# Performance work log

Measured on AMD Instinct MI355X. Metric: run time of the kernel, lower is better.

## Reference

```python
import jax, jax.numpy as jnp
import numpy as np

B, S, E = 8, 2048, 1024
H, DK = 128, 8  # embed_dim = H * DK; DK = n_wires per quantum head


def setup_inputs() -> dict:
    key = jax.random.key(0)
    k1, k2, k3, k4 = jax.random.split(key, 4)
    x = jax.random.normal(k1, (B, S, E), dtype=jnp.float32)
    theta = jax.random.normal(k2, (H, DK), dtype=jnp.float32)  # trainable RX angles per head/wire
    W = jax.random.normal(k3, (E, E), dtype=jnp.float32) * (1.0 / np.sqrt(E))
    b = jax.random.normal(k4, (E,), dtype=jnp.float32) * 0.01
    return {"x": x, "theta": theta, "W": W, "b": b}


def reference(x, theta, W, b):
    # Quantum circuit per token/head: RX(x_i) then RX(theta_i) on wire i starting
    # from |0...0>. Single-qubit RX gates compose: RX(a)RX(b)=RX(a+b), and
    # <Z> after RX(angle)|0> = cos(angle). So the MeasureAll(PauliZ) output is
    # cos(x_i + theta_i) elementwise -- fully vectorized over batch/seq/head/wire.
    Bx, Sx, Ex = x.shape
    Hx, dk = theta.shape
    xs = x.reshape(Bx, Sx, Hx, dk)            # [B,S,H,dk]
    head_out = jnp.cos(xs + theta[None, None])  # [B,S,H,dk]
    out = head_out.reshape(Bx, Sx, Ex)
    return out @ W.T + b                       # combine Linear
```

## Files before the change

### kernel.cpp

```cpp
#include <hip/hip_runtime.h>
#include <hip/hip_bf16.h>
#include <stdint.h>

#define M_DIM 16384
#define N_DIM 1024
#define K_DIM 1024

typedef __attribute__((ext_vector_type(8))) short short8;
typedef __attribute__((ext_vector_type(4))) float f32x4;

#define GLD_LDS(g, l) __builtin_amdgcn_global_load_lds( \
    (const __attribute__((address_space(1))) unsigned int*)(g), \
    (__attribute__((address_space(3))) unsigned int*)(l), 16, 0, 0)

__device__ __forceinline__ unsigned short f2bf(float f) {
  union { float f; unsigned int u; } v;
  v.f = f;
  unsigned int u = v.u + 0x7FFFu + ((v.u >> 16) & 1u);
  return (unsigned short)(u >> 16);
}

#define PREP_A_BLOCKS (M_DIM * K_DIM / (256 * 8))
#define PREP_W_BLOCKS (N_DIM * K_DIM / (256 * 8))
__global__ __launch_bounds__(256) void prep_all(const float* __restrict__ x,
                                                const float* __restrict__ theta,
                                                const float* __restrict__ W,
                                                unsigned short* __restrict__ A,
                                                unsigned short* __restrict__ Wb) {
  if (blockIdx.x < PREP_A_BLOCKS) {
    const long i = ((long)blockIdx.x * 256 + threadIdx.x) * 8;
    const int k = (int)(i & (K_DIM - 1));
    float4 x0 = *(const float4*)(x + i);
    float4 x1 = *(const float4*)(x + i + 4);
    float4 t0 = *(const float4*)(theta + k);
    float4 t1 = *(const float4*)(theta + k + 4);
    union { unsigned short s[8]; short8 v; } o;
    o.s[0] = f2bf(__cosf(x0.x + t0.x));
    o.s[1] = f2bf(__cosf(x0.y + t0.y));
    o.s[2] = f2bf(__cosf(x0.z + t0.z));
    o.s[3] = f2bf(__cosf(x0.w + t0.w));
    o.s[4] = f2bf(__cosf(x1.x + t1.x));
    o.s[5] = f2bf(__cosf(x1.y + t1.y));
    o.s[6] = f2bf(__cosf(x1.z + t1.z));
    o.s[7] = f2bf(__cosf(x1.w + t1.w));
    *(short8*)(A + i) = o.v;
  } else {
    const long i = ((long)(blockIdx.x - PREP_A_BLOCKS) * 256 + threadIdx.x) * 8;
    float4 w0 = *(const float4*)(W + i);
    float4 w1 = *(const float4*)(W + i + 4);
    union { unsigned short s[8]; short8 v; } o;
    o.s[0] = f2bf(w0.x); o.s[1] = f2bf(w0.y); o.s[2] = f2bf(w0.z); o.s[3] = f2bf(w0.w);
    o.s[4] = f2bf(w1.x); o.s[5] = f2bf(w1.y); o.s[6] = f2bf(w1.z); o.s[7] = f2bf(w1.w);
    *(short8*)(Wb + i) = o.v;
  }
}

__global__ __launch_bounds__(512, 2) void gemm_bt(const unsigned short* __restrict__ A,
                                                  const unsigned short* __restrict__ Bt,
                                                  const float* __restrict__ bias,
                                                  float* __restrict__ C) {
  constexpr int NTT = K_DIM / 64;
  __shared__ unsigned short As[4 * 8192];
  __shared__ unsigned short Bs[4 * 8192];
  const int tid = threadIdx.x;

  const int L = blockIdx.y * 4 + blockIdx.x;
  const int xcd = L & 7;
  const int idx = L >> 3;
  const int by = xcd * 8 + (idx >> 2);
  const int bx = idx & 3;
  const int m0 = by * 256;
  const int n0 = bx * 256;

  const int lane = tid & 63;
  const int wave = tid >> 6;
  const int wm = (wave >> 2) * 128;
  const int wn = (wave & 3) * 64;
  const int fr = lane & 15;
  const int fq = lane >> 4;

  f32x4 acc[8][4] = {};

  const int srow = ((tid >> 5) << 3) | (tid & 7);
  const int kc = (tid >> 3) & 3;
  const unsigned short* AgU = A + (long)(m0 + srow) * K_DIM + kc * 8;
  const unsigned short* BgU = Bt + (long)(n0 + srow) * K_DIM + kc * 8;
  unsigned short* AsD = As + tid * 8;
  unsigned short* BsD = Bs + tid * 8;

#define STAGE_A(UNIT, TAU, KH) do { \
    const unsigned short* g_ = AgU + (TAU) * 64 + (KH) * 32; \
    unsigned short* d_ = AsD + (UNIT) * 8192; \
    GLD_LDS(g_, d_); \
    GLD_LDS(g_ + (long)128 * K_DIM, d_ + 4096); \
  } while (0)
#define STAGE_B(UNIT, TAU, KH) do { \
    const unsigned short* g_ = BgU + (TAU) * 64 + (KH) * 32; \
    unsigned short* d_ = BsD + (UNIT) * 8192; \
    GLD_LDS(g_, d_); \
    GLD_LDS(g_ + (long)128 * K_DIM, d_ + 4096); \
  } while (0)

  const int baseA = ((wm >> 3) + (fr >> 3)) * 256 + fq * 64 + (fr & 7) * 8;
  const int baseB = ((wn >> 3) + (fr >> 3)) * 256 + fq * 64 + (fr & 7) * 8;

  short8 bf0, bf1, bf2, bf3;

#define MFMA16(IH, A0, A1, A2, A3) do { \
    __builtin_amdgcn_s_setprio(1); \
    acc[(IH)*4+0][0] = __builtin_amdgcn_mfma_f32_16x16x32_bf16(A0, bf0, acc[(IH)*4+0][0], 0, 0, 0); \
    acc[(IH)*4+0][1] = __builtin_amdgcn_mfma_f32_16x16x32_bf16(A0, bf1, acc[(IH)*4+0][1], 0, 0, 0); \
    acc[(IH)*4+0][2] = __builtin_amdgcn_mfma_f32_16x16x32_bf16(A0, bf2, acc[(IH)*4+0][2], 0, 0, 0); \
    acc[(IH)*4+0][3] = __builtin_amdgcn_mfma_f32_16x16x32_bf16(A0, bf3, acc[(IH)*4+0][3], 0, 0, 0); \
    acc[(IH)*4+1][0] = __builtin_amdgcn_mfma_f32_16x16x32_bf16(A1, bf0, acc[(IH)*4+1][0], 0, 0, 0); \
    acc[(IH)*4+1][1] = __builtin_amdgcn_mfma_f32_16x16x32_bf16(A1, bf1, acc[(IH)*4+1][1], 0, 0, 0); \
    acc[(IH)*4+1][2] = __builtin_amdgcn_mfma_f32_16x16x32_bf16(A1, bf2, acc[(IH)*4+1][2], 0, 0, 0); \
    acc[(IH)*4+1][3] = __builtin_amdgcn_mfma_f32_16x16x32_bf16(A1, bf3, acc[(IH)*4+1][3], 0, 0, 0); \
    acc[(IH)*4+2][0] = __builtin_amdgcn_mfma_f32_16x16x32_bf16(A2, bf0, acc[(IH)*4+2][0], 0, 0, 0); \
    acc[(IH)*4+2][1] = __builtin_amdgcn_mfma_f32_16x16x32_bf16(A2, bf1, acc[(IH)*4+2][1], 0, 0, 0); \
    acc[(IH)*4+2][2] = __builtin_amdgcn_mfma_f32_16x16x32_bf16(A2, bf2, acc[(IH)*4+2][2], 0, 0, 0); \
    acc[(IH)*4+2][3] = __builtin_amdgcn_mfma_f32_16x16x32_bf16(A2, bf3, acc[(IH)*4+2][3], 0, 0, 0); \
    acc[(IH)*4+3][0] = __builtin_amdgcn_mfma_f32_16x16x32_bf16(A3, bf0, acc[(IH)*4+3][0], 0, 0, 0); \
    acc[(IH)*4+3][1] = __builtin_amdgcn_mfma_f32_16x16x32_bf16(A3, bf1, acc[(IH)*4+3][1], 0, 0, 0); \
    acc[(IH)*4+3][2] = __builtin_amdgcn_mfma_f32_16x16x32_bf16(A3, bf2, acc[(IH)*4+3][2], 0, 0, 0); \
    acc[(IH)*4+3][3] = __builtin_amdgcn_mfma_f32_16x16x32_bf16(A3, bf3, acc[(IH)*4+3][3], 0, 0, 0); \
    __builtin_amdgcn_s_setprio(0); \
  } while (0)

#define BAR() do { asm volatile("" ::: "memory"); __builtin_amdgcn_s_barrier(); \
                   asm volatile("" ::: "memory"); } while (0)
#define VMW(N) asm volatile("s_waitcnt vmcnt(" #N ")" ::: "memory")

#define PHASE_LO(Au, Bu, ISSUE, WAIT) do { \
    BAR(); \
    ISSUE; \
    bf0 = *(const short8*)((Bu) + baseB + 0); \
    bf1 = *(const short8*)((Bu) + baseB + 512); \
    bf2 = *(const short8*)((Bu) + baseB + 1024); \
    bf3 = *(const short8*)((Bu) + baseB + 1536); \
    { short8 a0 = *(const short8*)((Au) + baseA + 0); \
      short8 a1 = *(const short8*)((Au) + baseA + 512); \
      short8 a2 = *(const short8*)((Au) + baseA + 1024); \
      short8 a3 = *(const short8*)((Au) + baseA + 1536); \
      MFMA16(0, a0, a1, a2, a3); } \
    WAIT; \
  } while (0)

#define PHASE_HI(Au, ISSUE, WAIT) do { \
    BAR(); \
    ISSUE; \
    { short8 a0 = *(const short8*)((Au) + baseA + 2048); \
      short8 a1 = *(const short8*)((Au) + baseA + 2560); \
      short8 a2 = *(const short8*)((Au) + baseA + 3072); \
      short8 a3 = *(const short8*)((Au) + baseA + 3584); \
      MFMA16(1, a0, a1, a2, a3); } \
    WAIT; \
  } while (0)

  STAGE_A(0, 0, 0);
  STAGE_B(0, 0, 0);
  STAGE_A(1, 0, 1);
  STAGE_B(1, 0, 1);
  STAGE_A(2, 1, 0);
  STAGE_B(2, 1, 0);
  VMW(8);

  for (int t = 0; t < NTT - 2; ++t) {
    const int db = t & 1;
    const int u0 = db * 2;
    const int u1 = db * 2 + 1;
    const int v1 = (db ^ 1) * 2 + 1;
    const unsigned short* Au0 = As + u0 * 8192;
    const unsigned short* Bu0 = Bs + u0 * 8192;
    const unsigned short* Au1 = As + u1 * 8192;
    const unsigned short* Bu1 = Bs + u1 * 8192;
    PHASE_LO(Au0, Bu0, STAGE_A(v1, t + 1, 1), (void)0);
    PHASE_HI(Au0,      STAGE_B(v1, t + 1, 1), VMW(8));
    PHASE_LO(Au1, Bu1, STAGE_A(u0, t + 2, 0), (void)0);
    PHASE_HI(Au1,      STAGE_B(u0, t + 2, 0), VMW(8));
  }
  {
    const unsigned short* Au0 = As;
    const unsigned short* Bu0 = Bs;
    const unsigned short* Au1 = As + 8192;
    const unsigned short* Bu1 = Bs + 8192;
    PHASE_LO(Au0, Bu0, STAGE_A(3, 15, 1), (void)0);
    PHASE_HI(Au0,      STAGE_B(3, 15, 1), VMW(8));
    PHASE_LO(Au1, Bu1, (void)0,           (void)0);
    PHASE_HI(Au1,      (void)0,           VMW(4));
  }
  {
    const unsigned short* Au0 = As + 2 * 8192;
    const unsigned short* Bu0 = Bs + 2 * 8192;
    const unsigned short* Au1 = As + 3 * 8192;
    const unsigned short* Bu1 = Bs + 3 * 8192;
    PHASE_LO(Au0, Bu0, (void)0, (void)0);
    PHASE_HI(Au0,      (void)0, VMW(0));
    PHASE_LO(Au1, Bu1, (void)0, (void)0);
    PHASE_HI(Au1,      (void)0, (void)0);
  }

  const int cn = lane & 15;
  const int rq = (lane >> 4) * 4;
#pragma unroll
  for (int j = 0; j < 4; ++j) {
    const int n = n0 + wn + j * 16 + cn;
    const float bv = bias[n];
#pragma unroll
    for (int i = 0; i < 8; ++i) {
      const long mb = (long)(m0 + wm + i * 16 + rq) * N_DIM + n;
#pragma unroll
      for (int r = 0; r < 4; ++r)
        C[mb + (long)r * N_DIM] = acc[i][j][r] + bv;
    }
  }
}

extern "C" void kernel_launch(void* const* d_in, const int* in_sizes, int n_in,
                              void* d_out, int out_size, void* d_ws, size_t ws_size,
                              hipStream_t stream) {
  const float* x = (const float*)d_in[0];
  const float* theta = (const float*)d_in[1];
  const float* W = (const float*)d_in[2];
  const float* b = (const float*)d_in[3];
  float* out = (float*)d_out;

  unsigned short* Abf = (unsigned short*)d_ws;
  unsigned short* Wbf = Abf + (size_t)M_DIM * K_DIM;

  hipLaunchKernelGGL(prep_all, dim3(PREP_A_BLOCKS + PREP_W_BLOCKS), dim3(256), 0,
                     stream, x, theta, W, Abf, Wbf);
  hipLaunchKernelGGL(gemm_bt, dim3(N_DIM / 256, M_DIM / 256), dim3(512), 0, stream,
                     Abf, Wbf, b, out);
}
```

Before: 160.0 us.

## Issue LDS fragment reads before barrier and reorder B/A staging

Each phase now reads its A/B fragments from LDS and issues the next global-to-LDS stage before the workgroup barrier, then waits on lgkmcnt and runs the MFMAs after the barrier. The aim is to overlap LDS read latency with barrier wait and keep memory traffic flowing. The staging order is swapped so B is issued before A, which changes which buffer the vmcnt waits cover. This reorders the read/write hazards across buffers, so correctness depends on the staged buffer not aliasing the one being read in the same phase.

```diff
diff --git a/kernel.cpp b/kernel.cpp
--- a/kernel.cpp
+++ b/kernel.cpp
@@ -130,40 +130,45 @@
 #define BAR() do { asm volatile("" ::: "memory"); __builtin_amdgcn_s_barrier(); \
                    asm volatile("" ::: "memory"); } while (0)
 #define VMW(N) asm volatile("s_waitcnt vmcnt(" #N ")" ::: "memory")
-
-#define PHASE_LO(Au, Bu, ISSUE, WAIT) do { \
-    BAR(); \
-    ISSUE; \
+#define LGKM0() do { asm volatile("s_waitcnt lgkmcnt(0)" ::: "memory"); \
+                     __builtin_amdgcn_sched_barrier(0); } while (0)
+
+#define PHASE_LO(Au, Bu, ISSUE, WAITPRE) do { \
     bf0 = *(const short8*)((Bu) + baseB + 0); \
     bf1 = *(const short8*)((Bu) + baseB + 512); \
     bf2 = *(const short8*)((Bu) + baseB + 1024); \
     bf3 = *(const short8*)((Bu) + baseB + 1536); \
-    { short8 a0 = *(const short8*)((Au) + baseA + 0); \
-      short8 a1 = *(const short8*)((Au) + baseA + 512); \
-      short8 a2 = *(const short8*)((Au) + baseA + 1024); \
-      short8 a3 = *(const short8*)((Au) + baseA + 1536); \
-      MFMA16(0, a0, a1, a2, a3); } \
-    WAIT; \
-  } while (0)
-
-#define PHASE_HI(Au, ISSUE, WAIT) do { \
+    short8 a0 = *(const short8*)((Au) + baseA + 0); \
+    short8 a1 = *(const short8*)((Au) + baseA + 512); \
+    short8 a2 = *(const short8*)((Au) + baseA + 1024); \
+    short8 a3 = *(const short8*)((Au) + baseA + 1536); \
+    ISSUE; \
+    WAITPRE; \
     BAR(); \
+    LGKM0(); \
+    MFMA16(0, a0, a1, a2, a3); \
+  } while (0)
+
+#define PHASE_HI(Au, ISSUE, WAITPRE) do { \
+    short8 a0 = *(const short8*)((Au) + baseA + 2048); \
+    short8 a1 = *(const short8*)((Au) + baseA + 2560); \
+    short8 a2 = *(const short8*)((Au) + baseA + 3072); \
+    short8 a3 = *(const short8*)((Au) + baseA + 3584); \
     ISSUE; \
-    { short8 a0 = *(const short8*)((Au) + baseA + 2048); \
-      short8 a1 = *(const short8*)((Au) + baseA + 2560); \
-      short8 a2 = *(const short8*)((Au) + baseA + 3072); \
-      short8 a3 = *(const short8*)((Au) + baseA + 3584); \
-      MFMA16(1, a0, a1, a2, a3); } \
-    WAIT; \
-  } while (0)
-
+    WAITPRE; \
+    BAR(); \
+    LGKM0(); \
+    MFMA16(1, a0, a1, a2, a3); \
+  } while (0)
+
+  STAGE_B(0, 0, 0);
   STAGE_A(0, 0, 0);
-  STAGE_B(0, 0, 0);
+  STAGE_B(1, 0, 1);
   STAGE_A(1, 0, 1);
-  STAGE_B(1, 0, 1);
+  STAGE_B(2, 1, 0);
   STAGE_A(2, 1, 0);
-  STAGE_B(2, 1, 0);
   VMW(8);
+  BAR();
 
   for (int t = 0; t < NTT - 2; ++t) {
     const int db = t & 1;
@@ -174,18 +179,18 @@
     const unsigned short* Bu0 = Bs + u0 * 8192;
     const unsigned short* Au1 = As + u1 * 8192;
     const unsigned short* Bu1 = Bs + u1 * 8192;
-    PHASE_LO(Au0, Bu0, STAGE_A(v1, t + 1, 1), (void)0);
-    PHASE_HI(Au0,      STAGE_B(v1, t + 1, 1), VMW(8));
-    PHASE_LO(Au1, Bu1, STAGE_A(u0, t + 2, 0), (void)0);
-    PHASE_HI(Au1,      STAGE_B(u0, t + 2, 0), VMW(8));
+    PHASE_LO(Au0, Bu0, STAGE_B(v1, t + 1, 1), (void)0);
+    PHASE_HI(Au0,      STAGE_A(v1, t + 1, 1), VMW(8));
+    PHASE_LO(Au1, Bu1, STAGE_B(u0, t + 2, 0), (void)0);
+    PHASE_HI(Au1,      STAGE_A(u0, t + 2, 0), VMW(8));
   }
   {
     const unsigned short* Au0 = As;
     const unsigned short* Bu0 = Bs;
     const unsigned short* Au1 = As + 8192;
     const unsigned short* Bu1 = Bs + 8192;
-    PHASE_LO(Au0, Bu0, STAGE_A(3, 15, 1), (void)0);
-    PHASE_HI(Au0,      STAGE_B(3, 15, 1), VMW(8));
+    PHASE_LO(Au0, Bu0, STAGE_B(3, 15, 1), (void)0);
+    PHASE_HI(Au0,      STAGE_A(3, 15, 1), VMW(8));
     PHASE_LO(Au1, Bu1, (void)0,           (void)0);
     PHASE_HI(Au1,      (void)0,           VMW(4));
   }
```

New measurement: 155.7 us. 2.7% less time.
